# Performance work log

Measured on AMD Instinct MI355X. Metric: run time of the kernel, lower is better.

## Reference

```python
import jax, jax.numpy as jnp
import numpy as np

B, S, E, H = 2, 2048, 1024, 16
D = E // H  # head_dim = 64


def setup_inputs() -> dict:
    key = jax.random.key(0)
    ks = jax.random.split(key, 8)
    lim = float(np.sqrt(6.0 / (E + E)))  # xavier_uniform
    inp = {
        "query": jax.random.normal(ks[0], (B, S, E), jnp.float32),
        "key": jax.random.normal(ks[1], (B, S, E), jnp.float32),
        "value": jax.random.normal(ks[2], (B, S, E), jnp.float32),
        "Wq": jax.random.uniform(ks[3], (E, E), jnp.float32, -lim, lim),
        "Wk": jax.random.uniform(ks[4], (E, E), jnp.float32, -lim, lim),
        "Wv": jax.random.uniform(ks[5], (E, E), jnp.float32, -lim, lim),
        "Wo": jax.random.uniform(ks[6], (E, E), jnp.float32, -lim, lim),
        "bq": jnp.zeros((E,), jnp.float32),
        "bk": jnp.zeros((E,), jnp.float32),
        "bv": jnp.zeros((E,), jnp.float32),
        "bo": jnp.zeros((E,), jnp.float32),
        # causal mask: True = masked (strictly upper triangular)
        "attn_mask": jnp.triu(jnp.ones((S, S), jnp.bool_), k=1),
    }
    return inp


def reference(query, key, value, Wq, Wk, Wv, Wo, bq, bk, bv, bo, attn_mask):
    # W stored as (in, out); torch Linear equivalent y = x @ W + b
    scaling = D ** (-0.5)
    q = (query @ Wq + bq) * scaling            # (B,S,E), first scaling (MHA.forward)
    k = key @ Wk + bk
    v = value @ Wv + bv
    # split heads -> (B, H, S, D)
    q = q.reshape(B, S, H, D).transpose(0, 2, 1, 3)
    k = k.reshape(B, S, H, D).transpose(0, 2, 1, 3)
    v = v.reshape(B, S, H, D).transpose(0, 2, 1, 3)
    # second scaling inside ScaledDotProductAttention (faithful double-scale)
    scores = jnp.einsum("bhqd,bhkd->bhqk", q, k) / jnp.sqrt(jnp.float32(D))
    scores = jnp.where(attn_mask[None, None, :, :], -jnp.inf, scores)
    attn = jax.nn.softmax(scores, axis=-1)     # dropout is identity in eval
    out = jnp.einsum("bhqk,bhkd->bhqd", attn, v)
    out = out.transpose(0, 2, 1, 3).reshape(B, S, E)
    return out @ Wo + bo
```

## Files before the change

### kernel.cpp

```cpp
#include <hip/hip_runtime.h>
#include <stdint.h>

#define B_ 2
#define S_ 2048
#define E_ 1024
#define H_ 16
#define D_ 64

typedef __attribute__((ext_vector_type(8))) short bf16x8;
typedef __attribute__((ext_vector_type(4))) float f32x4;
typedef __attribute__((ext_vector_type(4))) short s16x4_t;

__device__ __forceinline__ short bfbits(float x) {
    union { float f; uint32_t u; } v; v.f = x;
    uint32_t r = v.u + 0x7fffu + ((v.u >> 16) & 1u);
    return (short)(r >> 16);
}
__device__ __forceinline__ short bfbits_trunc(float x) {
    union { float f; uint32_t u; } v; v.f = x;
    return (short)(v.u >> 16);
}

__device__ __forceinline__ void async16(const short* g, short* l) {
    __builtin_amdgcn_global_load_lds((const __attribute__((address_space(1))) void*)g,
                                     (__attribute__((address_space(3))) void*)l,
                                     16, 0, 0);
}

__global__ __launch_bounds__(256) void cvt_inputs(const float* __restrict__ q,
                                                  const float* __restrict__ k,
                                                  const float* __restrict__ v,
                                                  short* __restrict__ dst) {
    const long long NV = 1048576;
    long long i = (long long)blockIdx.x * 256 + threadIdx.x;
    const float* src = (i < NV) ? q : (i < 2 * NV) ? k : v;
    long long j = (i >= 2 * NV) ? (i - 2 * NV) : (i >= NV) ? (i - NV) : i;
    float4 x = ((const float4*)src)[j];
    s16x4_t o;
    o[0] = bfbits(x.x); o[1] = bfbits(x.y); o[2] = bfbits(x.z); o[3] = bfbits(x.w);
    ((s16x4_t*)dst)[i] = o;
}

__global__ __launch_bounds__(256) void cvt_wT(const float* __restrict__ Wq,
                                              const float* __restrict__ Wk,
                                              const float* __restrict__ Wv,
                                              const float* __restrict__ Wo,
                                              short* __restrict__ dst) {
    __shared__ short t[64][72];
    int z = blockIdx.z;
    const float* W = (z == 0) ? Wq : (z == 1) ? Wk : (z == 2) ? Wv : Wo;
    short* o = dst + (size_t)z * 1048576;
    int n0 = blockIdx.x * 64, k0 = blockIdx.y * 64;
    int tid = threadIdx.x;
    int r = tid >> 4, c4 = tid & 15;
    for (int rep = 0; rep < 4; rep++) {
        int kk = rep * 16 + r;
        float4 x = *(const float4*)&W[(size_t)(k0 + kk) * 1024 + n0 + c4 * 4];
        t[c4 * 4 + 0][kk] = bfbits(x.x);
        t[c4 * 4 + 1][kk] = bfbits(x.y);
        t[c4 * 4 + 2][kk] = bfbits(x.z);
        t[c4 * 4 + 3][kk] = bfbits(x.w);
    }
    __syncthreads();
    int n = tid >> 3, c8 = tid & 7;
    for (int rep = 0; rep < 2; rep++) {
        int nn = rep * 32 + n;
        bf16x8 vv;
        for (int jj = 0; jj < 8; jj++) vv[jj] = t[nn][c8 * 8 + jj];
        *(bf16x8*)&o[(size_t)(n0 + nn) * 1024 + k0 + c8 * 8] = vv;
    }
}

__device__ __forceinline__ void gemm_core(const short* __restrict__ A,
                                          const short* __restrict__ Bt,
                                          const float* __restrict__ bias,
                                          short* __restrict__ outB,
                                          float* __restrict__ outF,
                                          int mode, float scale) {
    __shared__ short As[128 * 64];
    __shared__ short Bs[128 * 64];
    int tid = threadIdx.x, lane = tid & 63, w = tid >> 6;
    int col = lane & 15, quad = lane >> 4;
    int m0 = blockIdx.y * 128, n0 = blockIdx.x * 128;
    int wm = (w >> 1) * 64, wn = (w & 1) * 64;
    f32x4 acc[4][4];
    for (int i = 0; i < 4; i++)
        for (int j = 0; j < 4; j++) acc[i][j] = (f32x4){0.f, 0.f, 0.f, 0.f};

    int r8 = lane >> 3;
    int sk = ((lane & 7) ^ r8) * 8;
    int c7 = col & 7;

    for (int k0 = 0; k0 < 1024; k0 += 64) {
        for (int c = 0; c < 4; c++) {
            int rb = w * 32 + c * 8;
            async16(A + (size_t)(m0 + rb + r8) * 1024 + k0 + sk, &As[rb * 64]);
            async16(Bt + (size_t)(n0 + rb + r8) * 1024 + k0 + sk, &Bs[rb * 64]);
        }
        __syncthreads();
        for (int ks = 0; ks < 2; ks++) {
            bf16x8 af[4], bfr[4];
            int sl = ((ks * 4 + quad) ^ c7) * 8;
            for (int i = 0; i < 4; i++)
                af[i] = *(const bf16x8*)&As[(wm + i * 16 + col) * 64 + sl];
            for (int j = 0; j < 4; j++)
                bfr[j] = *(const bf16x8*)&Bs[(wn + j * 16 + col) * 64 + sl];
            for (int i = 0; i < 4; i++)
                for (int j = 0; j < 4; j++)
                    acc[i][j] = __builtin_amdgcn_mfma_f32_16x16x32_bf16(af[i], bfr[j], acc[i][j], 0, 0, 0);
        }
        __syncthreads();
    }

    int mbase = m0 + wm + quad * 4;
    for (int i = 0; i < 4; i++) {
        int mb = mbase + i * 16;
        for (int j = 0; j < 4; j++) {
            int n = n0 + wn + j * 16 + col;
            float bv_ = bias[n];
            if (mode == 0) {
                for (int r = 0; r < 4; r++)
                    outB[(size_t)(mb + r) * 1024 + n] = bfbits((acc[i][j][r] + bv_) * scale);
            } else if (mode == 1) {
                int b_ = mb >> 11, s_ = mb & 2047;
                size_t base = (((size_t)(b_ * 16 + (n >> 6)) * 64) + (n & 63)) * 2048 + s_;
                s16x4_t pv;
                for (int r = 0; r < 4; r++) pv[r] = bfbits((acc[i][j][r] + bv_) * scale);
                *(s16x4_t*)&outB[base] = pv;
            } else {
                for (int r = 0; r < 4; r++)
                    outF[(size_t)(mb + r) * 1024 + n] = (acc[i][j][r] + bv_) * scale;
            }
        }
    }
}

#define QSCALE (0.015625f * 1.44269504088896340736f)
__global__ __launch_bounds__(256) void gemm_qkv(const short* __restrict__ Xb,
                                                const short* __restrict__ Wb,
                                                const float* __restrict__ bq,
                                                const float* __restrict__ bk,
                                                const float* __restrict__ bv,
                                                short* __restrict__ Qp) {
    int z = blockIdx.z;
    const short* A = Xb + (size_t)z * 4194304;
    const short* Bt = Wb + (size_t)z * 1048576;
    const float* bias = (z == 0) ? bq : (z == 1) ? bk : bv;
    short* outB = Qp + (size_t)z * 4194304;
    gemm_core(A, Bt, bias, outB, nullptr, (z == 2) ? 1 : 0, (z == 0) ? QSCALE : 1.0f);
}

__global__ __launch_bounds__(256) void gemm_o(const short* __restrict__ Ctx,
                                              const short* __restrict__ Wob,
                                              const float* __restrict__ bo,
                                              float* __restrict__ out) {
    gemm_core(Ctx, Wob, bo, nullptr, out, 2, 1.0f);
}

__device__ __forceinline__ void stage_kv(const short* __restrict__ Kp,
                                         const short* __restrict__ VpT,
                                         short* Kbuf, short* Vbuf,
                                         int b, int bh, int h, int kv0,
                                         int lane, int w) {
    int r8 = lane >> 3;
    int sk = ((lane & 7) ^ r8) * 8;
    for (int c = 0; c < 2; c++) {
        int rb = (c * 4 + w) * 8;
        async16(Kp + (size_t)(b * 2048 + kv0 + rb + r8) * 1024 + h * 64 + sk,
                &Kbuf[rb * 64]);
        async16(VpT + (size_t)(bh * 64 + rb + r8) * 2048 + kv0 + sk,
                &Vbuf[rb * 64]);
    }
}

__global__ __launch_bounds__(256) void attn_kernel(const short* __restrict__ Qp,
                                                   const short* __restrict__ Kp,
                                                   const short* __restrict__ VpT,
                                                   short* __restrict__ Ctx) {
    __shared__ short Kt[2][64 * 64];
    __shared__ short Vt[2][64 * 64];
    __shared__ short Pl[4][16 * 72];
    int tid = threadIdx.x, lane = tid & 63, w = tid >> 6;
    int col = lane & 15, quad = lane >> 4;
    int c7 = col & 7;
    int bh = blockIdx.y, b = bh >> 4, h = bh & 15;

    for (int half = 0; half < 2; half++) {
        int qt = half ? (31 - blockIdx.x) : blockIdx.x;
        int qrow = qt * 64 + w * 16;

        bf16x8 aq0, aq1;
        {
            const short* qa = Qp + ((size_t)(b * 2048 + qrow + col)) * 1024 + h * 64;
            aq0 = *(const bf16x8*)(qa + quad * 8);
            aq1 = *(const bf16x8*)(qa + 32 + quad * 8);
        }
        f32x4 o[4];
        for (int dj = 0; dj < 4; dj++) o[dj] = (f32x4){0.f, 0.f, 0.f, 0.f};
        float psum = 0.f;

        int n = qt + 1;
        if (half) __syncthreads();
        stage_kv(Kp, VpT, Kt[0], Vt[0], b, bh, h, 0, lane, w);

        for (int t = 0; t < n; t++) {
            __syncthreads();
            if (t + 1 < n)
                stage_kv(Kp, VpT, Kt[(t + 1) & 1], Vt[(t + 1) & 1], b, bh, h,
                         (t + 1) * 64, lane, w);
            const short* Kb = Kt[t & 1];
            const short* Vb = Vt[t & 1];

            f32x4 sf[4];
            for (int i = 0; i < 4; i++) sf[i] = (f32x4){0.f, 0.f, 0.f, 0.f};
            for (int ks = 0; ks < 2; ks++) {
                bf16x8 bq_ = ks ? aq1 : aq0;
                int sl = ((ks * 4 + quad) ^ c7) * 8;
                for (int i = 0; i < 4; i++) {
                    bf16x8 ak_ = *(const bf16x8*)&Kb[(i * 16 + col) * 64 + sl];
                    sf[i] = __builtin_amdgcn_mfma_f32_16x16x32_bf16(ak_, bq_, sf[i], 0, 0, 0);
                }
            }
            if (t == n - 1) {
                int qg = qrow + col;
                for (int i = 0; i < 4; i++) {
                    int kvg = t * 64 + i * 16 + quad * 4;
                    for (int r = 0; r < 4; r++)
                        if (kvg + r > qg) sf[i][r] = -3.0e38f;
                }
            }
            for (int i = 0; i < 4; i++) {
                s16x4_t pw;
                for (int r = 0; r < 4; r++) {
                    float p = exp2f(sf[i][r]);
                    psum += p;
                    pw[r] = bfbits_trunc(p);
                }
                *(s16x4_t*)&Pl[w][col * 72 + i * 16 + quad * 4] = pw;
            }
            for (int ks = 0; ks < 2; ks++) {
                bf16x8 ap = *(const bf16x8*)&Pl[w][col * 72 + ks * 32 + quad * 8];
                int sl = ((ks * 4 + quad) ^ c7) * 8;
                for (int dj = 0; dj < 4; dj++) {
                    bf16x8 bv_ = *(const bf16x8*)&Vb[(dj * 16 + col) * 64 + sl];
                    o[dj] = __builtin_amdgcn_mfma_f32_16x16x32_bf16(ap, bv_, o[dj], 0, 0, 0);
                }
            }
        }
        psum += __shfl_xor(psum, 16);
        psum += __shfl_xor(psum, 32);
        float inv[4];
        for (int r = 0; r < 4; r++) inv[r] = 1.0f / __shfl(psum, quad * 4 + r);
        for (int r = 0; r < 4; r++) {
            for (int dj = 0; dj < 4; dj++) {
                float val = o[dj][r] * inv[r];
                Ctx[((size_t)(b * 2048 + qrow + quad * 4 + r)) * 1024 + h * 64 + dj * 16 + col] = bfbits(val);
            }
        }
    }
}

extern "C" void kernel_launch(void* const* d_in, const int* in_sizes, int n_in,
                              void* d_out, int out_size, void* d_ws, size_t ws_size,
                              hipStream_t stream) {
    const float* q  = (const float*)d_in[0];
    const float* k  = (const float*)d_in[1];
    const float* v  = (const float*)d_in[2];
    const float* Wq = (const float*)d_in[3];
    const float* Wk = (const float*)d_in[4];
    const float* Wv = (const float*)d_in[5];
    const float* Wo = (const float*)d_in[6];
    const float* bq = (const float*)d_in[7];
    const float* bk = (const float*)d_in[8];
    const float* bv = (const float*)d_in[9];
    const float* bo = (const float*)d_in[10];

    short* wsb = (short*)d_ws;
    short* Wb  = wsb;
    short* Xb  = Wb + 4 * 1048576;
    short* Qp  = Xb + 3 * 4194304;
    short* Kp  = Qp + 4194304;
    short* VpT = Kp + 4194304;
    short* Ctx = VpT + 4194304;

    cvt_inputs<<<12288, 256, 0, stream>>>(q, k, v, Xb);
    cvt_wT<<<dim3(16, 16, 4), 256, 0, stream>>>(Wq, Wk, Wv, Wo, Wb);
    gemm_qkv<<<dim3(8, 32, 3), 256, 0, stream>>>(Xb, Wb, bq, bk, bv, Qp);
    attn_kernel<<<dim3(16, 32), 256, 0, stream>>>(Qp, Kp, VpT, Ctx);
    gemm_o<<<dim3(8, 32), 256, 0, stream>>>(Ctx, Wb + 3 * 1048576, bo, (float*)d_out);
}
```

Before: 248.3 us.

## Double-buffer GEMM K-loop, remap blocks for XCD locality, prioritize attention MFMA

The GEMM core switches from a single 64-wide K tile with two barriers per step to a double-buffered 32-wide K tile. The next tile's async global-to-LDS load is issued before the current tile's MFMAs, so load latency overlaps compute, and the XOR swizzle is adapted to the new tile width. GEMM launches become 1D grids with a block-index remap that groups neighbouring tiles onto the same XCD for better L2 reuse. The attention kernel wraps its MFMA sections in s_setprio to favour matrix issue across waves. The risk is that the smaller K step doubles the iteration count and barrier count.

```diff
diff --git a/kernel.cpp b/kernel.cpp
--- a/kernel.cpp
+++ b/kernel.cpp
@@ -76,39 +76,46 @@
                                           const float* __restrict__ bias,
                                           short* __restrict__ outB,
                                           float* __restrict__ outF,
-                                          int mode, float scale) {
-    __shared__ short As[128 * 64];
-    __shared__ short Bs[128 * 64];
+                                          int mode, float scale,
+                                          int m0, int n0) {
+    __shared__ short As[2][128 * 32];
+    __shared__ short Bs[2][128 * 32];
     int tid = threadIdx.x, lane = tid & 63, w = tid >> 6;
     int col = lane & 15, quad = lane >> 4;
-    int m0 = blockIdx.y * 128, n0 = blockIdx.x * 128;
     int wm = (w >> 1) * 64, wn = (w & 1) * 64;
     f32x4 acc[4][4];
     for (int i = 0; i < 4; i++)
         for (int j = 0; j < 4; j++) acc[i][j] = (f32x4){0.f, 0.f, 0.f, 0.f};
 
-    int r8 = lane >> 3;
-    int sk = ((lane & 7) ^ r8) * 8;
-    int c7 = col & 7;
-
-    for (int k0 = 0; k0 < 1024; k0 += 64) {
-        for (int c = 0; c < 4; c++) {
-            int rb = w * 32 + c * 8;
-            async16(A + (size_t)(m0 + rb + r8) * 1024 + k0 + sk, &As[rb * 64]);
-            async16(Bt + (size_t)(n0 + rb + r8) * 1024 + k0 + sk, &Bs[rb * 64]);
-        }
-        __syncthreads();
-        for (int ks = 0; ks < 2; ks++) {
-            bf16x8 af[4], bfr[4];
-            int sl = ((ks * 4 + quad) ^ c7) * 8;
-            for (int i = 0; i < 4; i++)
-                af[i] = *(const bf16x8*)&As[(wm + i * 16 + col) * 64 + sl];
+    int r4 = lane >> 2;
+    int skoff = ((lane & 3) ^ ((r4 >> 1) & 3)) * 8;
+    const short* ga = A + (size_t)(m0 + r4) * 1024 + skoff;
+    const short* gb = Bt + (size_t)(n0 + r4) * 1024 + skoff;
+
+    int fro = (quad ^ ((col >> 1) & 3)) * 8;
+
+    auto stage = [&](int t, int b) {
+        int k0_ = t * 32;
+        for (int c = 0; c < 2; ++c) {
+            int rb = w * 32 + c * 16;
+            async16(ga + (size_t)rb * 1024 + k0_, &As[b][rb * 32]);
+            async16(gb + (size_t)rb * 1024 + k0_, &Bs[b][rb * 32]);
+        }
+    };
+
+    stage(0, 0);
+    __syncthreads();
+    for (int t = 0; t < 32; ++t) {
+        int cur = t & 1;
+        if (t + 1 < 32) stage(t + 1, cur ^ 1);
+        bf16x8 af[4], bfr[4];
+        for (int i = 0; i < 4; i++)
+            af[i] = *(const bf16x8*)&As[cur][(wm + i * 16 + col) * 32 + fro];
+        for (int j = 0; j < 4; j++)
+            bfr[j] = *(const bf16x8*)&Bs[cur][(wn + j * 16 + col) * 32 + fro];
+        for (int i = 0; i < 4; i++)
             for (int j = 0; j < 4; j++)
-                bfr[j] = *(const bf16x8*)&Bs[(wn + j * 16 + col) * 64 + sl];
-            for (int i = 0; i < 4; i++)
-                for (int j = 0; j < 4; j++)
-                    acc[i][j] = __builtin_amdgcn_mfma_f32_16x16x32_bf16(af[i], bfr[j], acc[i][j], 0, 0, 0);
-        }
+                acc[i][j] = __builtin_amdgcn_mfma_f32_16x16x32_bf16(af[i], bfr[j], acc[i][j], 0, 0, 0);
         __syncthreads();
     }
 
@@ -142,19 +149,27 @@
                                                 const float* __restrict__ bk,
                                                 const float* __restrict__ bv,
                                                 short* __restrict__ Qp) {
-    int z = blockIdx.z;
+    int bid = blockIdx.x;
+    int L = (bid & 7) * 96 + (bid >> 3);
+    int z = L >> 8;
+    int rem = L & 255;
+    int m0 = (rem >> 3) * 128, n0 = (rem & 7) * 128;
     const short* A = Xb + (size_t)z * 4194304;
     const short* Bt = Wb + (size_t)z * 1048576;
     const float* bias = (z == 0) ? bq : (z == 1) ? bk : bv;
     short* outB = Qp + (size_t)z * 4194304;
-    gemm_core(A, Bt, bias, outB, nullptr, (z == 2) ? 1 : 0, (z == 0) ? QSCALE : 1.0f);
+    gemm_core(A, Bt, bias, outB, nullptr, (z == 2) ? 1 : 0, (z == 0) ? QSCALE : 1.0f,
+              m0, n0);
 }
 
 __global__ __launch_bounds__(256) void gemm_o(const short* __restrict__ Ctx,
                                               const short* __restrict__ Wob,
                                               const float* __restrict__ bo,
                                               float* __restrict__ out) {
-    gemm_core(Ctx, Wob, bo, nullptr, out, 2, 1.0f);
+    int bid = blockIdx.x;
+    int L = (bid & 7) * 32 + (bid >> 3);
+    int m0 = (L >> 3) * 128, n0 = (L & 7) * 128;
+    gemm_core(Ctx, Wob, bo, nullptr, out, 2, 1.0f, m0, n0);
 }
 
 __device__ __forceinline__ void stage_kv(const short* __restrict__ Kp,
@@ -213,6 +228,7 @@
 
             f32x4 sf[4];
             for (int i = 0; i < 4; i++) sf[i] = (f32x4){0.f, 0.f, 0.f, 0.f};
+            __builtin_amdgcn_s_setprio(1);
             for (int ks = 0; ks < 2; ks++) {
                 bf16x8 bq_ = ks ? aq1 : aq0;
                 int sl = ((ks * 4 + quad) ^ c7) * 8;
@@ -221,6 +237,7 @@
                     sf[i] = __builtin_amdgcn_mfma_f32_16x16x32_bf16(ak_, bq_, sf[i], 0, 0, 0);
                 }
             }
+            __builtin_amdgcn_s_setprio(0);
             if (t == n - 1) {
                 int qg = qrow + col;
                 for (int i = 0; i < 4; i++) {
@@ -238,6 +255,7 @@
                 }
                 *(s16x4_t*)&Pl[w][col * 72 + i * 16 + quad * 4] = pw;
             }
+            __builtin_amdgcn_s_setprio(1);
             for (int ks = 0; ks < 2; ks++) {
                 bf16x8 ap = *(const bf16x8*)&Pl[w][col * 72 + ks * 32 + quad * 8];
                 int sl = ((ks * 4 + quad) ^ c7) * 8;
@@ -246,6 +264,7 @@
                     o[dj] = __builtin_amdgcn_mfma_f32_16x16x32_bf16(ap, bv_, o[dj], 0, 0, 0);
                 }
             }
+            __builtin_amdgcn_s_setprio(0);
         }
         psum += __shfl_xor(psum, 16);
         psum += __shfl_xor(psum, 32);
@@ -285,7 +304,7 @@
 
     cvt_inputs<<<12288, 256, 0, stream>>>(q, k, v, Xb);
     cvt_wT<<<dim3(16, 16, 4), 256, 0, stream>>>(Wq, Wk, Wv, Wo, Wb);
-    gemm_qkv<<<dim3(8, 32, 3), 256, 0, stream>>>(Xb, Wb, bq, bk, bv, Qp);
+    gemm_qkv<<<768, 256, 0, stream>>>(Xb, Wb, bq, bk, bv, Qp);
     attn_kernel<<<dim3(16, 32), 256, 0, stream>>>(Qp, Kp, VpT, Ctx);
-    gemm_o<<<dim3(8, 32), 256, 0, stream>>>(Ctx, Wb + 3 * 1048576, bo, (float*)d_out);
-}
+    gemm_o<<<256, 256, 0, stream>>>(Ctx, Wb + 3 * 1048576, bo, (float*)d_out);
+}
```

New measurement: 242.5 us. 1.02x faster.
